# Kernel optimization log

Measured on AMD Instinct MI355X. Metric: run time of the kernel, lower is better.

## Reference

```python
import jax, jax.numpy as jnp
import numpy as np

N = 100_000   # nodes
E = 1_600_000 # edges (avg degree 16)
IN, H, C = 3, 32, 4
DIMS = [(IN, H), (H, 2 * H), (2 * H, 3 * H), (3 * H, 4 * H)]  # SAGEConv layer dims


def setup_inputs() -> dict:
    key = jax.random.key(0)
    ks = jax.random.split(key, 16)
    inp = {
        "x": jax.random.normal(ks[0], (N, IN), dtype=jnp.float32),
        "edge_index": jax.random.randint(ks[1], (2, E), 0, N, dtype=jnp.int32).astype(jnp.int64),
    }
    i = 2
    for l, (din, dout) in enumerate(DIMS):
        s = 1.0 / float(np.sqrt(din))
        inp[f"Wl{l}"] = jax.random.normal(ks[i], (din, dout), dtype=jnp.float32) * s; i += 1
        inp[f"bl{l}"] = jnp.zeros((dout,), jnp.float32)
        inp[f"Wr{l}"] = jax.random.normal(ks[i], (din, dout), dtype=jnp.float32) * s; i += 1
    sf = 1.0 / float(np.sqrt(4 * H))
    inp["Wf"] = jax.random.normal(ks[i], (4 * H, C), dtype=jnp.float32) * sf
    inp["bf"] = jnp.zeros((C,), jnp.float32)
    return inp


def _sage_conv(h, src, dst, Wl, bl, Wr):
    # PyG SAGEConv (aggr='mean'): lin_l(mean_{j in N(i)} x_j) + lin_r(x_i)
    n = h.shape[0]
    agg = jax.ops.segment_sum(h[src], dst, num_segments=n)            # [N, din]
    deg = jax.ops.segment_sum(jnp.ones((src.shape[0],), h.dtype), dst, num_segments=n)
    mean = agg / jnp.maximum(deg, 1.0)[:, None]
    return mean @ Wl + bl + h @ Wr


def reference(x, edge_index, Wl0, bl0, Wr0, Wl1, bl1, Wr1, Wl2, bl2, Wr2, Wl3, bl3, Wr3, Wf, bf):
    src, dst = edge_index[0], edge_index[1]
    h = x
    for Wl, bl, Wr in ((Wl0, bl0, Wr0), (Wl1, bl1, Wr1), (Wl2, bl2, Wr2), (Wl3, bl3, Wr3)):
        h = jax.nn.relu(_sage_conv(h, src, dst, Wl, bl, Wr))
    return jax.nn.sigmoid(h @ Wf + bf)  # [N, class_num]
```

## Files before the change

kernel.cpp:

```cpp
#include <hip/hip_runtime.h>
#include <math.h>

#define NN 100000
#define NE 1600000
#define BUCKETS ((NN + 255) >> 8)
#define RVPT 16

typedef short bf16x8 __attribute__((ext_vector_type(8)));
typedef float f32x4 __attribute__((ext_vector_type(4)));

__device__ inline float bsf(unsigned short u) { return __uint_as_float(((unsigned)u) << 16); }
__device__ inline unsigned short f2bs(float f) {
    unsigned u = __float_as_uint(f);
    return (unsigned short)((u + 0x7fffu + ((u >> 16) & 1u)) >> 16);
}

__global__ __launch_bounds__(256) void bhist_k(const int* __restrict__ dst,
                                               int* __restrict__ bhist) {
    __shared__ int bh[BUCKETS];
    for (int i = threadIdx.x; i < BUCKETS; i += 256) bh[i] = 0;
    __syncthreads();
    int e0 = blockIdx.x * (256 * RVPT) + threadIdx.x;
#pragma unroll
    for (int v = 0; v < RVPT; ++v) {
        int e = e0 + v * 256;
        if (e < NE) atomicAdd(&bh[dst[e] >> 8], 1);
    }
    __syncthreads();
    for (int i = threadIdx.x; i < BUCKETS; i += 256)
        if (bh[i]) atomicAdd(&bhist[i], bh[i]);
}

__global__ __launch_bounds__(512) void bscan_k(const int* __restrict__ bhist,
                                               int* __restrict__ bcur) {
    __shared__ int buf[512];
    int tid = threadIdx.x;
    int v = (tid < BUCKETS) ? bhist[tid] : 0;
    buf[tid] = v;
    __syncthreads();
    for (int off = 1; off < 512; off <<= 1) {
        int t = (tid >= off) ? buf[tid - off] : 0;
        __syncthreads();
        buf[tid] += t;
        __syncthreads();
    }
    if (tid < BUCKETS) bcur[tid] = buf[tid] - v;
}

__global__ __launch_bounds__(256) void reorder_k(const int* __restrict__ src,
                                                 const int* __restrict__ dst,
                                                 int* __restrict__ bcur,
                                                 unsigned long long* __restrict__ ebuf) {
    __shared__ int hist[BUCKETS];
    __shared__ int base[BUCKETS];
    int tid = threadIdx.x;
    for (int i = tid; i < BUCKETS; i += 256) hist[i] = 0;
    __syncthreads();
    int e0 = blockIdx.x * (256 * RVPT) + tid;
    unsigned long long pair[RVPT];
    int pr[RVPT];
#pragma unroll
    for (int v = 0; v < RVPT; ++v) {
        int e = e0 + v * 256;
        if (e < NE) {
            int s = src[e], d = dst[e];
            pair[v] = ((unsigned long long)(unsigned)d << 32) | (unsigned)s;
            int b = d >> 8;
            int r = atomicAdd(&hist[b], 1);
            pr[v] = (b << 12) | r;
        } else pr[v] = -1;
    }
    __syncthreads();
    for (int i = tid; i < BUCKETS; i += 256)
        base[i] = hist[i] ? atomicAdd(&bcur[i], hist[i]) : 0;
    __syncthreads();
#pragma unroll
    for (int v = 0; v < RVPT; ++v) {
        if (pr[v] >= 0) {
            int b = pr[v] >> 12, r = pr[v] & 4095;
            ebuf[(size_t)base[b] + r] = pair[v];
        }
    }
}

__global__ __launch_bounds__(256) void pcsr_k(const unsigned long long* __restrict__ ebuf,
                                              const int* __restrict__ bend,
                                              int* __restrict__ row_ptr,
                                              int* __restrict__ col) {
    __shared__ int hist[256];
    __shared__ int wsum[4];
    int b = blockIdx.x;
    int tid = threadIdx.x;
    int beg = b ? bend[b - 1] : 0;
    int end = bend[b];

    hist[tid] = 0;
    __syncthreads();
    for (int e = beg + tid; e < end; e += 256)
        atomicAdd(&hist[(int)(ebuf[e] >> 32) & 255], 1);
    __syncthreads();

    int v = hist[tid];
    int lane = tid & 63, wid = tid >> 6;
    int s = v;
#pragma unroll
    for (int off = 1; off < 64; off <<= 1) {
        int t = __shfl_up(s, off);
        if (lane >= off) s += t;
    }
    if (lane == 63) wsum[wid] = s;
    __syncthreads();
    int prev = 0;
#pragma unroll
    for (int w = 0; w < 4; ++w) prev += (w < wid) ? wsum[w] : 0;
    int excl = beg + prev + s - v;

    int node = b * 256 + tid;
    if (node < NN) row_ptr[node] = excl;
    if (node == NN - 1) row_ptr[NN] = excl + v;

    hist[tid] = excl;
    __syncthreads();
    for (int e = beg + tid; e < end; e += 256) {
        unsigned long long p = ebuf[e];
        int d = (int)(p >> 32);
        int pos = atomicAdd(&hist[d & 255], 1);
        col[pos] = (int)(p & 0xffffffffu);
    }
}

template<int DIN, int DOUT>
__global__ void wcvt_k(const float* __restrict__ Wl, const float* __restrict__ Wr,
                       unsigned short* __restrict__ Wt) {
    int idx = blockIdx.x * 256 + threadIdx.x;
    if (idx < DOUT * 2 * DIN) {
        int j = idx / (2 * DIN), k = idx - j * 2 * DIN;
        float v = (k < DIN) ? Wl[(size_t)k * DOUT + j] : Wr[(size_t)(k - DIN) * DOUT + j];
        Wt[idx] = f2bs(v);
    }
}

__global__ __launch_bounds__(256) void agg0_k(const int* __restrict__ rp, const int* __restrict__ col,
                                              const float* __restrict__ x, unsigned short* __restrict__ magg) {
    int node = blockIdx.x * 4 + (threadIdx.x >> 6);
    int lane = threadIdx.x & 63;
    int fl = lane & 3, es = lane >> 2;
    int beg = rp[node], end = rp[node + 1];
    float acc = 0.0f;
    for (int e = beg + es; e < end; e += 16) {
        int idx = col[e];
        if (fl < 3) acc += x[(size_t)idx * 3 + fl];
    }
    acc += __shfl(acc, lane + 32);
    acc += __shfl(acc, lane + 16);
    acc += __shfl(acc, lane + 8);
    acc += __shfl(acc, lane + 4);
    if (lane < 3) {
        float inv = 1.0f / fmaxf((float)(end - beg), 1.0f);
        magg[(size_t)node * 3 + lane] = f2bs(acc * inv);
    }
}

template<int DIN, int FL, int EPW>
__global__ __launch_bounds__(256) void agg_k(const int* __restrict__ rp, const int* __restrict__ col,
                                             const unsigned short* __restrict__ hb,
                                             unsigned short* __restrict__ magg) {
    int node = blockIdx.x * 4 + (threadIdx.x >> 6);
    int lane = threadIdx.x & 63;
    int fl = lane % FL;
    int es = lane / FL;
    int beg = rp[node], end = rp[node + 1];

    float a[8];
#pragma unroll
    for (int i = 0; i < 8; ++i) a[i] = 0.0f;

    if (es < EPW) {
        int e = beg + es;
        for (; e + EPW < end; e += 2 * EPW) {
            uint4 v0 = *(const uint4*)(hb + (size_t)col[e]       * DIN + fl * 8);
            uint4 v1 = *(const uint4*)(hb + (size_t)col[e + EPW] * DIN + fl * 8);
            const unsigned short* p0 = (const unsigned short*)&v0;
            const unsigned short* p1 = (const unsigned short*)&v1;
#pragma unroll
            for (int i = 0; i < 8; ++i) a[i] += bsf(p0[i]) + bsf(p1[i]);
        }
        if (e < end) {
            uint4 v0 = *(const uint4*)(hb + (size_t)col[e] * DIN + fl * 8);
            const unsigned short* p0 = (const unsigned short*)&v0;
#pragma unroll
            for (int i = 0; i < 8; ++i) a[i] += bsf(p0[i]);
        }
    }

    if constexpr (FL == 4) {
#pragma unroll
        for (int i = 0; i < 8; ++i) {
            a[i] += __shfl(a[i], lane + 4);
            a[i] += __shfl(a[i], lane + 8);
            a[i] += __shfl(a[i], lane + 16);
            a[i] += __shfl(a[i], lane + 32);
        }
    } else if constexpr (FL == 8) {
#pragma unroll
        for (int i = 0; i < 8; ++i) {
            a[i] += __shfl(a[i], lane + 8);
            a[i] += __shfl(a[i], lane + 16);
            a[i] += __shfl(a[i], lane + 32);
        }
    } else {
#pragma unroll
        for (int i = 0; i < 8; ++i) {
            float g4 = __shfl(a[i], lane + 48);
            a[i] += __shfl(a[i], lane + 12);
            a[i] += __shfl(a[i], lane + 24);
            a[i] += g4;
        }
    }

    if (lane < FL) {
        float inv = 1.0f / fmaxf((float)(end - beg), 1.0f);
        unsigned short o[8];
#pragma unroll
        for (int i = 0; i < 8; ++i) o[i] = f2bs(a[i] * inv);
        *(uint4*)(magg + (size_t)node * DIN + fl * 8) = *(const uint4*)o;
    }
}

template<int DIN, int DOUT, int CT, bool FINAL, bool L0>
__global__ __launch_bounds__(256) void gemm_k(
    const unsigned short* __restrict__ magg, const void* __restrict__ hin,
    const float* __restrict__ Wl, const float* __restrict__ bl, const float* __restrict__ Wr,
    const float* __restrict__ Wf, const float* __restrict__ bfi,
    unsigned short* __restrict__ hout, float* __restrict__ out)
{
    __shared__ float sm[32][DIN + 1];
    __shared__ float sh[32][DIN + 1];

    int tx = threadIdx.x;
    int base = blockIdx.x * 32;

    const float* hx = (const float*)hin;
    for (int f = tx; f < 32 * 3; f += 256) {
        int n = f / 3, k = f - n * 3;
        sm[n][k] = bsf(magg[(size_t)(base + n) * 3 + k]);
        sh[n][k] = hx[(size_t)(base + n) * 3 + k];
    }
    __syncthreads();

    int ng = tx >> 5, cg = tx & 31;
    float acc[4][CT];
#pragma unroll
    for (int m = 0; m < 4; ++m)
#pragma unroll
        for (int c = 0; c < CT; ++c) acc[m][c] = bl[cg * CT + c];

#pragma unroll
    for (int k = 0; k < 3; ++k) {
        float wl[CT], wr[CT];
#pragma unroll
        for (int c = 0; c < CT; ++c) {
            wl[c] = Wl[(size_t)k * DOUT + cg * CT + c];
            wr[c] = Wr[(size_t)k * DOUT + cg * CT + c];
        }
#pragma unroll
        for (int m = 0; m < 4; ++m) {
            float mv = sm[ng * 4 + m][k];
            float hv = sh[ng * 4 + m][k];
#pragma unroll
            for (int c = 0; c < CT; ++c)
                acc[m][c] = fmaf(mv, wl[c], fmaf(hv, wr[c], acc[m][c]));
        }
    }

#pragma unroll
    for (int m = 0; m < 4; ++m)
#pragma unroll
        for (int c = 0; c < CT; ++c) {
            float v = fmaxf(acc[m][c], 0.0f);
            hout[(size_t)(base + ng * 4 + m) * DOUT + cg * CT + c] = f2bs(v);
        }
}

template<int DIN, int DOUT, bool FINAL>
__global__ __launch_bounds__(256) void mgemm_k(
    const unsigned short* __restrict__ magg, const unsigned short* __restrict__ h,
    const unsigned short* __restrict__ Wt, const float* __restrict__ bl,
    const float* __restrict__ Wf, const float* __restrict__ bfi,
    unsigned short* __restrict__ hout, float* __restrict__ out)
{
    constexpr int K2  = 2 * DIN;
    constexpr int STR = K2 + 8;
    constexpr int NT  = DOUT / 16;
    constexpr int KS  = K2 / 32;
    __shared__ unsigned short lA[64 * STR];
    __shared__ unsigned short lB[DOUT * STR];

    int tx = threadIdx.x;
    int base = blockIdx.x * 64;

    constexpr int CPM = DIN / 8;
    for (int c = tx; c < 64 * CPM; c += 256) {
        int n = c / CPM, o = (c - n * CPM) * 8;
        int node = base + n;
        uint4 vm = make_uint4(0, 0, 0, 0), vh = vm;
        if (node < NN) {
            vm = *(const uint4*)(magg + (size_t)node * DIN + o);
            vh = *(const uint4*)(h    + (size_t)node * DIN + o);
        }
        *(uint4*)(lA + n * STR + o)       = vm;
        *(uint4*)(lA + n * STR + DIN + o) = vh;
    }
    constexpr int CPW = K2 / 8;
    for (int c = tx; c < DOUT * CPW; c += 256) {
        int j = c / CPW, o = (c - j * CPW) * 8;
        *(uint4*)(lB + j * STR + o) = *(const uint4*)(Wt + (size_t)j * K2 + o);
    }
    __syncthreads();

    int lane = tx & 63;
    int wm = tx >> 6;
    int r16 = lane & 15, kg = lane >> 4;

    f32x4 acc[NT];
#pragma unroll
    for (int t = 0; t < NT; ++t) acc[t] = (f32x4){0.0f, 0.0f, 0.0f, 0.0f};

#pragma unroll
    for (int kk = 0; kk < KS; ++kk) {
        bf16x8 a = *(const bf16x8*)(lA + (wm * 16 + r16) * STR + kk * 32 + kg * 8);
#pragma unroll
        for (int t = 0; t < NT; ++t) {
            bf16x8 b = *(const bf16x8*)(lB + (t * 16 + r16) * STR + kk * 32 + kg * 8);
            acc[t] = __builtin_amdgcn_mfma_f32_16x16x32_bf16(a, b, acc[t], 0, 0, 0);
        }
    }

    if (!FINAL) {
#pragma unroll
        for (int t = 0; t < NT; ++t)
#pragma unroll
            for (int r = 0; r < 4; ++r) {
                int node = base + wm * 16 + kg * 4 + r;
                int colj = t * 16 + r16;
                float v = fmaxf(acc[t][r] + bl[colj], 0.0f);
                if (node < NN) hout[(size_t)node * DOUT + colj] = f2bs(v);
            }
    } else {
        __syncthreads();
        float* s4 = (float*)lB;
#pragma unroll
        for (int t = 0; t < NT; ++t)
#pragma unroll
            for (int r = 0; r < 4; ++r) {
                int nl = wm * 16 + kg * 4 + r;
                int colj = t * 16 + r16;
                s4[nl * 129 + colj] = fmaxf(acc[t][r] + bl[colj], 0.0f);
            }
        __syncthreads();
        int nl = tx >> 2, c = tx & 3;
        int node = base + nl;
        if (node < NN) {
            float a = bfi[c];
#pragma unroll 8
            for (int k = 0; k < 128; ++k)
                a = fmaf(s4[nl * 129 + k], Wf[k * 4 + c], a);
            out[(size_t)node * 4 + c] = 1.0f / (1.0f + expf(-a));
        }
    }
}

extern "C" void kernel_launch(void* const* d_in, const int* in_sizes, int n_in,
                              void* d_out, int out_size, void* d_ws, size_t ws_size,
                              hipStream_t stream) {
    const float* x   = (const float*)d_in[0];
    const int*   ei  = (const int*)d_in[1];
    const int*   src = ei;
    const int*   dst = ei + NE;
    const float* Wl0 = (const float*)d_in[2];
    const float* bl0 = (const float*)d_in[3];
    const float* Wr0 = (const float*)d_in[4];
    const float* Wl1 = (const float*)d_in[5];
    const float* bl1 = (const float*)d_in[6];
    const float* Wr1 = (const float*)d_in[7];
    const float* Wl2 = (const float*)d_in[8];
    const float* bl2 = (const float*)d_in[9];
    const float* Wr2 = (const float*)d_in[10];
    const float* Wl3 = (const float*)d_in[11];
    const float* bl3 = (const float*)d_in[12];
    const float* Wr3 = (const float*)d_in[13];
    const float* Wf  = (const float*)d_in[14];
    const float* bf  = (const float*)d_in[15];
    float* out = (float*)d_out;

    size_t ints = (size_t)(NN + 2) + 512 + 512 + NE;
    ints = (ints + 15) & ~(size_t)15;
    size_t need = ints * 4 + (size_t)NN * (96 + 32 + 64 + 96) * 2
                + (size_t)(64 * 64 + 96 * 128 + 128 * 192) * 2;
    if (ws_size < need) return;

    int* row_ptr = (int*)d_ws;
    int* bhist   = row_ptr + NN + 2;
    int* bcur    = bhist + 512;
    int* col     = bcur + 512;
    unsigned short* magg = (unsigned short*)((char*)d_ws + ints * 4);
    unsigned long long* ebuf = (unsigned long long*)magg;
    unsigned short* h1   = magg + (size_t)NN * 96;
    unsigned short* h2   = h1 + (size_t)NN * 32;
    unsigned short* h3   = h2 + (size_t)NN * 64;
    unsigned short* wt1  = h3 + (size_t)NN * 96;
    unsigned short* wt2  = wt1 + 64 * 64;
    unsigned short* wt3  = wt2 + 96 * 128;

    wcvt_k<32, 64><<<(64 * 64 + 255) / 256, 256, 0, stream>>>(Wl1, Wr1, wt1);
    wcvt_k<64, 96><<<(96 * 128 + 255) / 256, 256, 0, stream>>>(Wl2, Wr2, wt2);
    wcvt_k<96, 128><<<(128 * 192 + 255) / 256, 256, 0, stream>>>(Wl3, Wr3, wt3);

    hipMemsetAsync(bhist, 0, 512 * sizeof(int), stream);
    const int EB = (NE + 256 * RVPT - 1) / (256 * RVPT);
    bhist_k<<<EB, 256, 0, stream>>>(dst, bhist);
    bscan_k<<<1, 512, 0, stream>>>(bhist, bcur);
    reorder_k<<<EB, 256, 0, stream>>>(src, dst, bcur, ebuf);
    pcsr_k<<<BUCKETS, 256, 0, stream>>>(ebuf, bcur, row_ptr, col);

    const int AGRID = NN / 4;
    const int MG    = (NN + 63) / 64;

    agg0_k<<<AGRID, 256, 0, stream>>>(row_ptr, col, x, magg);
    gemm_k<3, 32, 1, false, true><<<NN / 32, 256, 0, stream>>>(
        magg, x, Wl0, bl0, Wr0, nullptr, nullptr, h1, nullptr);

    agg_k<32, 4, 16><<<AGRID, 256, 0, stream>>>(row_ptr, col, h1, magg);
    mgemm_k<32, 64, false><<<MG, 256, 0, stream>>>(
        magg, h1, wt1, bl1, nullptr, nullptr, h2, nullptr);

    agg_k<64, 8, 8><<<AGRID, 256, 0, stream>>>(row_ptr, col, h2, magg);
    mgemm_k<64, 96, false><<<MG, 256, 0, stream>>>(
        magg, h2, wt2, bl2, nullptr, nullptr, h3, nullptr);

    agg_k<96, 12, 5><<<AGRID, 256, 0, stream>>>(row_ptr, col, h3, magg);
    mgemm_k<96, 128, true><<<MG, 256, 0, stream>>>(
        magg, h3, wt3, bl3, Wf, bf, nullptr, out);
}
```

Measured before the change: 305.3 us.

## Tune CSR build parallelism, fuse weight conversion, use 32-bit gather offsets

Reduces edges per thread in the histogram and reorder kernels so more blocks run. Doubles the pcsr block size to 512 threads, keeping the 256-bin scan on the first half. Merges the three weight-conversion launches into one kernel. Switches gather address math in the aggregation kernels to 32-bit offsets. Smaller RVPT means more blocks and more global atomics on the bucket counters.

New measurement: 381.7 us. 25.0% more time.

```diff
diff --git a/kernel.cpp b/kernel.cpp
--- a/kernel.cpp
+++ b/kernel.cpp
@@ -4,7 +4,7 @@
 #define NN 100000
 #define NE 1600000
 #define BUCKETS ((NN + 255) >> 8)
-#define RVPT 16
+#define RVPT 4
 
 typedef short bf16x8 __attribute__((ext_vector_type(8)));
 typedef float f32x4 __attribute__((ext_vector_type(4)));
@@ -83,7 +83,7 @@
     }
 }
 
-__global__ __launch_bounds__(256) void pcsr_k(const unsigned long long* __restrict__ ebuf,
+__global__ __launch_bounds__(512) void pcsr_k(const unsigned long long* __restrict__ ebuf,
                                               const int* __restrict__ bend,
                                               int* __restrict__ row_ptr,
                                               int* __restrict__ col) {
@@ -94,34 +94,40 @@
     int beg = b ? bend[b - 1] : 0;
     int end = bend[b];
 
-    hist[tid] = 0;
-    __syncthreads();
-    for (int e = beg + tid; e < end; e += 256)
+    if (tid < 256) hist[tid] = 0;
+    __syncthreads();
+    for (int e = beg + tid; e < end; e += 512)
         atomicAdd(&hist[(int)(ebuf[e] >> 32) & 255], 1);
     __syncthreads();
 
-    int v = hist[tid];
-    int lane = tid & 63, wid = tid >> 6;
-    int s = v;
-#pragma unroll
-    for (int off = 1; off < 64; off <<= 1) {
-        int t = __shfl_up(s, off);
-        if (lane >= off) s += t;
-    }
-    if (lane == 63) wsum[wid] = s;
-    __syncthreads();
-    int prev = 0;
-#pragma unroll
-    for (int w = 0; w < 4; ++w) prev += (w < wid) ? wsum[w] : 0;
-    int excl = beg + prev + s - v;
-
-    int node = b * 256 + tid;
-    if (node < NN) row_ptr[node] = excl;
-    if (node == NN - 1) row_ptr[NN] = excl + v;
-
-    hist[tid] = excl;
-    __syncthreads();
-    for (int e = beg + tid; e < end; e += 256) {
+    int v = 0, excl = 0;
+    if (tid < 256) {
+        v = hist[tid];
+        int lane = tid & 63, wid = tid >> 6;
+        int s = v;
+#pragma unroll
+        for (int off = 1; off < 64; off <<= 1) {
+            int t = __shfl_up(s, off);
+            if (lane >= off) s += t;
+        }
+        if (lane == 63) wsum[wid] = s;
+        excl = s - v;
+    }
+    __syncthreads();
+    if (tid < 256) {
+        int wid = tid >> 6;
+        int prev = 0;
+#pragma unroll
+        for (int w = 0; w < 4; ++w) prev += (w < wid) ? wsum[w] : 0;
+        excl += beg + prev;
+        int node = b * 256 + tid;
+        if (node < NN) row_ptr[node] = excl;
+        if (node == NN - 1) row_ptr[NN] = excl + v;
+    }
+    __syncthreads();
+    if (tid < 256) hist[tid] = excl;
+    __syncthreads();
+    for (int e = beg + tid; e < end; e += 512) {
         unsigned long long p = ebuf[e];
         int d = (int)(p >> 32);
         int pos = atomicAdd(&hist[d & 255], 1);
@@ -129,14 +135,27 @@
     }
 }
 
-template<int DIN, int DOUT>
-__global__ void wcvt_k(const float* __restrict__ Wl, const float* __restrict__ Wr,
-                       unsigned short* __restrict__ Wt) {
+__global__ __launch_bounds__(256) void wcvt_all_k(
+    const float* __restrict__ Wl1, const float* __restrict__ Wr1,
+    const float* __restrict__ Wl2, const float* __restrict__ Wr2,
+    const float* __restrict__ Wl3, const float* __restrict__ Wr3,
+    unsigned short* __restrict__ wt1, unsigned short* __restrict__ wt2,
+    unsigned short* __restrict__ wt3) {
     int idx = blockIdx.x * 256 + threadIdx.x;
-    if (idx < DOUT * 2 * DIN) {
-        int j = idx / (2 * DIN), k = idx - j * 2 * DIN;
-        float v = (k < DIN) ? Wl[(size_t)k * DOUT + j] : Wr[(size_t)(k - DIN) * DOUT + j];
-        Wt[idx] = f2bs(v);
+    if (idx < 4096) {
+        int j = idx >> 6, k = idx & 63;
+        float v = (k < 32) ? Wl1[k * 64 + j] : Wr1[(k - 32) * 64 + j];
+        wt1[idx] = f2bs(v);
+    } else if (idx < 16384) {
+        int t = idx - 4096;
+        int j = t / 128, k = t - j * 128;
+        float v = (k < 64) ? Wl2[k * 96 + j] : Wr2[(k - 64) * 96 + j];
+        wt2[t] = f2bs(v);
+    } else if (idx < 40960) {
+        int t = idx - 16384;
+        int j = t / 192, k = t - j * 192;
+        float v = (k < 96) ? Wl3[k * 128 + j] : Wr3[(k - 96) * 128 + j];
+        wt3[t] = f2bs(v);
     }
 }
 
@@ -148,8 +167,8 @@
     int beg = rp[node], end = rp[node + 1];
     float acc = 0.0f;
     for (int e = beg + es; e < end; e += 16) {
-        int idx = col[e];
-        if (fl < 3) acc += x[(size_t)idx * 3 + fl];
+        unsigned off = (unsigned)(col[e] * 3);
+        if (fl < 3) acc += x[off + fl];
     }
     acc += __shfl(acc, lane + 32);
     acc += __shfl(acc, lane + 16);
@@ -178,15 +197,18 @@
     if (es < EPW) {
         int e = beg + es;
         for (; e + EPW < end; e += 2 * EPW) {
-            uint4 v0 = *(const uint4*)(hb + (size_t)col[e]       * DIN + fl * 8);
-            uint4 v1 = *(const uint4*)(hb + (size_t)col[e + EPW] * DIN + fl * 8);
+            unsigned o0 = (unsigned)(col[e]       * DIN);
+            unsigned o1 = (unsigned)(col[e + EPW] * DIN);
+            uint4 v0 = *(const uint4*)(hb + o0 + fl * 8);
+            uint4 v1 = *(const uint4*)(hb + o1 + fl * 8);
             const unsigned short* p0 = (const unsigned short*)&v0;
             const unsigned short* p1 = (const unsigned short*)&v1;
 #pragma unroll
             for (int i = 0; i < 8; ++i) a[i] += bsf(p0[i]) + bsf(p1[i]);
         }
         if (e < end) {
-            uint4 v0 = *(const uint4*)(hb + (size_t)col[e] * DIN + fl * 8);
+            unsigned o0 = (unsigned)(col[e] * DIN);
+            uint4 v0 = *(const uint4*)(hb + o0 + fl * 8);
             const unsigned short* p0 = (const unsigned short*)&v0;
 #pragma unroll
             for (int i = 0; i < 8; ++i) a[i] += bsf(p0[i]);
@@ -227,12 +249,11 @@
     }
 }
 
-template<int DIN, int DOUT, int CT, bool FINAL, bool L0>
+template<int DIN, int DOUT, int CT>
 __global__ __launch_bounds__(256) void gemm_k(
-    const unsigned short* __restrict__ magg, const void* __restrict__ hin,
+    const unsigned short* __restrict__ magg, const float* __restrict__ hx,
     const float* __restrict__ Wl, const float* __restrict__ bl, const float* __restrict__ Wr,
-    const float* __restrict__ Wf, const float* __restrict__ bfi,
-    unsigned short* __restrict__ hout, float* __restrict__ out)
+    unsigned short* __restrict__ hout)
 {
     __shared__ float sm[32][DIN + 1];
     __shared__ float sh[32][DIN + 1];
@@ -240,7 +261,6 @@
     int tx = threadIdx.x;
     int base = blockIdx.x * 32;
 
-    const float* hx = (const float*)hin;
     for (int f = tx; f < 32 * 3; f += 256) {
         int n = f / 3, k = f - n * 3;
         sm[n][k] = bsf(magg[(size_t)(base + n) * 3 + k]);
@@ -412,23 +432,20 @@
     unsigned short* wt2  = wt1 + 64 * 64;
     unsigned short* wt3  = wt2 + 96 * 128;
 
-    wcvt_k<32, 64><<<(64 * 64 + 255) / 256, 256, 0, stream>>>(Wl1, Wr1, wt1);
-    wcvt_k<64, 96><<<(96 * 128 + 255) / 256, 256, 0, stream>>>(Wl2, Wr2, wt2);
-    wcvt_k<96, 128><<<(128 * 192 + 255) / 256, 256, 0, stream>>>(Wl3, Wr3, wt3);
+    wcvt_all_k<<<160, 256, 0, stream>>>(Wl1, Wr1, Wl2, Wr2, Wl3, Wr3, wt1, wt2, wt3);
 
     hipMemsetAsync(bhist, 0, 512 * sizeof(int), stream);
     const int EB = (NE + 256 * RVPT - 1) / (256 * RVPT);
     bhist_k<<<EB, 256, 0, stream>>>(dst, bhist);
     bscan_k<<<1, 512, 0, stream>>>(bhist, bcur);
     reorder_k<<<EB, 256, 0, stream>>>(src, dst, bcur, ebuf);
-    pcsr_k<<<BUCKETS, 256, 0, stream>>>(ebuf, bcur, row_ptr, col);
+    pcsr_k<<<BUCKETS, 512, 0, stream>>>(ebuf, bcur, row_ptr, col);
 
     const int AGRID = NN / 4;
     const int MG    = (NN + 63) / 64;
 
     agg0_k<<<AGRID, 256, 0, stream>>>(row_ptr, col, x, magg);
-    gemm_k<3, 32, 1, false, true><<<NN / 32, 256, 0, stream>>>(
-        magg, x, Wl0, bl0, Wr0, nullptr, nullptr, h1, nullptr);
+    gemm_k<3, 32, 1><<<NN / 32, 256, 0, stream>>>(magg, x, Wl0, bl0, Wr0, h1);
 
     agg_k<32, 4, 16><<<AGRID, 256, 0, stream>>>(row_ptr, col, h1, magg);
     mgemm_k<32, 64, false><<<MG, 256, 0, stream>>>(
```
